# Optimization experiments

Hardware: AMD Instinct MI355X
Metric: run time of the kernel (lower is better)

Reference implementation:

```python
import jax, jax.numpy as jnp
import numpy as np


def _moving_avg(x, k):
    # Replicate-pad along channel/time axis C, then stride-1 mean window of size k.
    B, C, H, W = x.shape
    p = (k - 1) // 2
    xf = x.reshape(B, C, H * W)
    front = jnp.repeat(xf[:, :1, :], p, axis=1)
    end = jnp.repeat(xf[:, -1:, :], p, axis=1)
    padded = jnp.concatenate([front, xf, end], axis=1)  # [B, C+2p, HW]
    # Windowed mean via exclusive cumsum: sum over window i..i+k-1 = cs[i+k]-cs[i]
    cs = jnp.cumsum(padded, axis=1)
    cs = jnp.concatenate([jnp.zeros_like(cs[:, :1, :]), cs], axis=1)  # [B, C+2p+1, HW]
    out = (cs[:, k:, :] - cs[:, :-k, :]) / k  # [B, C, HW] since k odd
    return out.reshape(B, C, H, W)


def _seasonality(x, period):
    # Mean over channels sharing the same phase (c mod period), broadcast back.
    # Requires C % period == 0 (groups equal-size, matching the torch loop).
    B, C, H, W = x.shape
    G = C // period
    xr = x.reshape(B, G, period, H, W)  # [b, group, phase, h, w]
    m = jnp.mean(xr, axis=1, keepdims=True)  # [B, 1, period, H, W]
    return jnp.broadcast_to(m, (B, G, period, H, W)).reshape(B, C, H, W)


def setup_inputs() -> dict:
    key = jax.random.key(0)
    x = jax.random.normal(key, (32, 336, 32, 32), dtype=jnp.float32)
    return {"x": x, "kernel_size": 25, "pe": 24}


def reference(x, kernel_size, pe):
    T = _moving_avg(x, kernel_size)          # trend
    xd = x - T                               # detrended
    S = _seasonality(xd, pe)                 # seasonal component
    R = xd - S                               # residual
    return (T, S, R)
```

## Files before the change

### kernel.cpp

```cpp
#include <hip/hip_runtime.h>


#define C_TOT 336
#define HWSZ 1024
#define PERIOD 24
#define GROUPS 14
#define PAD 12
#define W 32
#define SEG_C 12
#define NSEG 28
#define NTHREADS (NSEG * W)

__global__ __launch_bounds__(NTHREADS, 8) void decomp_kernel(
    const float* __restrict__ x,
    float* __restrict__ outT,
    float* __restrict__ outS,
    float* __restrict__ outR)
{
    __shared__ float sx[C_TOT][W];
    __shared__ float sv[PERIOD][W];

    const int tid = threadIdx.x;
    const int b   = blockIdx.y;
    const int hw0 = blockIdx.x * W;

    const float4* __restrict__ xg =
        (const float4*)(x + (size_t)b * C_TOT * HWSZ + hw0);
    float4* __restrict__ sx4 = (float4*)sx;
    #pragma unroll
    for (int k = 0; k < 3; ++k) {
        const int idx = tid + k * NTHREADS;
        sx4[idx] = xg[(idx >> 3) * (HWSZ / 4) + (idx & 7)];
    }
    __syncthreads();

    const int col = tid & (W - 1);
    const int seg = tid >> 5;
    const int c0  = seg * SEG_C;
    const float inv25 = 1.0f / 25.0f;
    const float inv14 = 1.0f / (float)GROUPS;

    const size_t base = (size_t)b * C_TOT * HWSZ + hw0 + col;
    float* __restrict__ Tb = outT + base;
    float* __restrict__ Sb = outS + base;
    float* __restrict__ Rb = outR + base;

    float wa = 0.0f, wb = 0.0f;
    #pragma unroll
    for (int d = -PAD; d <= PAD; d += 2) {
        int cc = c0 + d;
        cc = cc < 0 ? 0 : cc; cc = cc > C_TOT - 1 ? C_TOT - 1 : cc;
        wa += sx[cc][col];
    }
    #pragma unroll
    for (int d = -PAD + 1; d <= PAD; d += 2) {
        int cc = c0 + d;
        cc = cc < 0 ? 0 : cc; cc = cc > C_TOT - 1 ? C_TOT - 1 : cc;
        wb += sx[cc][col];
    }
    float winsum = wa + wb;

    float xd[SEG_C];
    #pragma unroll
    for (int j = 0; j < SEG_C; ++j) {
        const int c = c0 + j;
        const float tval = winsum * inv25;
        __builtin_nontemporal_store(tval, &Tb[(size_t)c * HWSZ]);
        xd[j] = sx[c][col] - tval;
        int chi = c + 1 + PAD; chi = chi > C_TOT - 1 ? C_TOT - 1 : chi;
        int clo = c - PAD;     clo = clo < 0 ? 0 : clo;
        winsum += sx[chi][col] - sx[clo][col];
    }
    __syncthreads();

    #pragma unroll
    for (int j = 0; j < SEG_C; ++j) sx[c0 + j][col] = xd[j];
    __syncthreads();

    if (tid < PERIOD * W) {
        const int p = tid >> 5, cc = tid & (W - 1);
        float s = 0.0f;
        #pragma unroll
        for (int g = 0; g < GROUPS; ++g) s += sx[g * PERIOD + p][cc];
        sv[p][cc] = s * inv14;
    }
    __syncthreads();

    const int pbase = (seg & 1) * SEG_C;
    #pragma unroll
    for (int j = 0; j < SEG_C; ++j) {
        const int c = c0 + j;
        const float s = sv[pbase + j][col];
        __builtin_nontemporal_store(s, &Sb[(size_t)c * HWSZ]);
        __builtin_nontemporal_store(xd[j] - s, &Rb[(size_t)c * HWSZ]);
    }
}

extern "C" void kernel_launch(void* const* d_in, const int* in_sizes, int n_in,
                              void* d_out, int out_size, void* d_ws, size_t ws_size,
                              hipStream_t stream) {
    const float* x = (const float*)d_in[0];
    float* out = (float*)d_out;
    const size_t N = (size_t)32 * C_TOT * HWSZ;

    dim3 grid(HWSZ / W, 32);
    decomp_kernel<<<grid, NTHREADS, 0, stream>>>(x, out, out + N, out + 2 * N);
}
```

Before: 174.7 us.

## Stream input from global in two passes instead of staging tile in LDS

Drops the 336x32 shared-memory tile and uses wider 128-column blocks with 4 channel segments. Each thread reads x directly from global memory in two passes: one computes the trend and accumulates per-phase detrended sums in shared memory, and a second recomputes the trend and writes the seasonal and residual outputs. This removes the large LDS footprint so more blocks can be resident per CU. The cost is re-reading the input from global/L2 several times over: three loads per channel per pass plus the window prologue.

```diff
diff --git a/kernel.cpp b/kernel.cpp
--- a/kernel.cpp
+++ b/kernel.cpp
@@ -1,98 +1,122 @@
 #include <hip/hip_runtime.h>
 
 
-#define C_TOT 336
-#define HWSZ 1024
-#define PERIOD 24
-#define GROUPS 14
-#define PAD 12
-#define W 32
-#define SEG_C 12
-#define NSEG 28
+#define C_TOT   336
+#define HWSZ    1024
+#define PERIOD  24
+#define GROUPS  14
+#define PAD     12
+#define KWIN    25
+#define W       128
+#define NSEG    4
+#define SEG_C   (C_TOT / NSEG)
 #define NTHREADS (NSEG * W)
+#define NCHUNK  12
+#define NU      (SEG_C / NCHUNK)
 
-__global__ __launch_bounds__(NTHREADS, 8) void decomp_kernel(
+__global__ __launch_bounds__(NTHREADS) void decomp_kernel(
     const float* __restrict__ x,
     float* __restrict__ outT,
     float* __restrict__ outS,
     float* __restrict__ outR)
 {
-    __shared__ float sx[C_TOT][W];
-    __shared__ float sv[PERIOD][W];
+    __shared__ float sv[NSEG][PERIOD][W];
+    __shared__ float sS[PERIOD][W];
 
     const int tid = threadIdx.x;
+    const int h   = tid & (W - 1);
+    const int s   = tid >> 7;
     const int b   = blockIdx.y;
     const int hw0 = blockIdx.x * W;
-
-    const float4* __restrict__ xg =
-        (const float4*)(x + (size_t)b * C_TOT * HWSZ + hw0);
-    float4* __restrict__ sx4 = (float4*)sx;
-    #pragma unroll
-    for (int k = 0; k < 3; ++k) {
-        const int idx = tid + k * NTHREADS;
-        sx4[idx] = xg[(idx >> 3) * (HWSZ / 4) + (idx & 7)];
-    }
-    __syncthreads();
-
-    const int col = tid & (W - 1);
-    const int seg = tid >> 5;
-    const int c0  = seg * SEG_C;
-    const float inv25 = 1.0f / 25.0f;
+    const int c0  = s * SEG_C;
+    const float inv25 = 1.0f / (float)KWIN;
     const float inv14 = 1.0f / (float)GROUPS;
 
-    const size_t base = (size_t)b * C_TOT * HWSZ + hw0 + col;
-    float* __restrict__ Tb = outT + base;
-    float* __restrict__ Sb = outS + base;
-    float* __restrict__ Rb = outR + base;
+    const size_t base = (size_t)b * C_TOT * HWSZ + hw0 + h;
+    const float* __restrict__ xb = x    + base;
+    float* __restrict__ Tb       = outT + base;
+    float* __restrict__ Sb       = outS + base;
+    float* __restrict__ Rb       = outR + base;
 
-    float wa = 0.0f, wb = 0.0f;
     #pragma unroll
-    for (int d = -PAD; d <= PAD; d += 2) {
-        int cc = c0 + d;
-        cc = cc < 0 ? 0 : cc; cc = cc > C_TOT - 1 ? C_TOT - 1 : cc;
-        wa += sx[cc][col];
-    }
-    #pragma unroll
-    for (int d = -PAD + 1; d <= PAD; d += 2) {
-        int cc = c0 + d;
-        cc = cc < 0 ? 0 : cc; cc = cc > C_TOT - 1 ? C_TOT - 1 : cc;
-        wb += sx[cc][col];
-    }
-    float winsum = wa + wb;
+    for (int p = 0; p < PERIOD; ++p) sv[s][p][h] = 0.0f;
 
-    float xd[SEG_C];
-    #pragma unroll
-    for (int j = 0; j < SEG_C; ++j) {
-        const int c = c0 + j;
-        const float tval = winsum * inv25;
-        __builtin_nontemporal_store(tval, &Tb[(size_t)c * HWSZ]);
-        xd[j] = sx[c][col] - tval;
-        int chi = c + 1 + PAD; chi = chi > C_TOT - 1 ? C_TOT - 1 : chi;
-        int clo = c - PAD;     clo = clo < 0 ? 0 : clo;
-        winsum += sx[chi][col] - sx[clo][col];
+    {
+        float winsum = 0.0f;
+        #pragma unroll
+        for (int d = -PAD; d <= PAD; ++d) {
+            int cc = c0 + d;
+            cc = cc < 0 ? 0 : (cc > C_TOT - 1 ? C_TOT - 1 : cc);
+            winsum += xb[(size_t)cc * HWSZ];
+        }
+        int p = (s & 1) * PAD;
+        for (int u = 0; u < NU; ++u) {
+            float lead[NCHUNK], xc[NCHUNK], trail[NCHUNK];
+            #pragma unroll
+            for (int i = 0; i < NCHUNK; ++i) {
+                const int c   = c0 + u * NCHUNK + i;
+                const int chi = (c + 1 + PAD > C_TOT - 1) ? C_TOT - 1 : c + 1 + PAD;
+                const int clo = (c - PAD < 0) ? 0 : c - PAD;
+                lead[i]  = xb[(size_t)chi * HWSZ];
+                trail[i] = xb[(size_t)clo * HWSZ];
+                xc[i]    = xb[(size_t)c   * HWSZ];
+            }
+            #pragma unroll
+            for (int i = 0; i < NCHUNK; ++i) {
+                const int c = c0 + u * NCHUNK + i;
+                const float tval = winsum * inv25;
+                const float xd   = xc[i] - tval;
+                __builtin_nontemporal_store(tval, &Tb[(size_t)c * HWSZ]);
+                sv[s][p][h] += xd;
+                winsum += lead[i] - trail[i];
+                p = (p == PERIOD - 1) ? 0 : p + 1;
+            }
+        }
     }
     __syncthreads();
 
     #pragma unroll
-    for (int j = 0; j < SEG_C; ++j) sx[c0 + j][col] = xd[j];
-    __syncthreads();
-
-    if (tid < PERIOD * W) {
-        const int p = tid >> 5, cc = tid & (W - 1);
-        float s = 0.0f;
-        #pragma unroll
-        for (int g = 0; g < GROUPS; ++g) s += sx[g * PERIOD + p][cc];
-        sv[p][cc] = s * inv14;
+    for (int k = 0; k < (PERIOD * W) / NTHREADS; ++k) {
+        const int idx = tid + k * NTHREADS;
+        const int pp  = idx >> 7;
+        const int hh  = idx & (W - 1);
+        sS[pp][hh] = (sv[0][pp][hh] + sv[1][pp][hh] +
+                      sv[2][pp][hh] + sv[3][pp][hh]) * inv14;
     }
     __syncthreads();
 
-    const int pbase = (seg & 1) * SEG_C;
-    #pragma unroll
-    for (int j = 0; j < SEG_C; ++j) {
-        const int c = c0 + j;
-        const float s = sv[pbase + j][col];
-        __builtin_nontemporal_store(s, &Sb[(size_t)c * HWSZ]);
-        __builtin_nontemporal_store(xd[j] - s, &Rb[(size_t)c * HWSZ]);
+    {
+        float winsum = 0.0f;
+        #pragma unroll
+        for (int d = -PAD; d <= PAD; ++d) {
+            int cc = c0 + d;
+            cc = cc < 0 ? 0 : (cc > C_TOT - 1 ? C_TOT - 1 : cc);
+            winsum += xb[(size_t)cc * HWSZ];
+        }
+        int p = (s & 1) * PAD;
+        for (int u = 0; u < NU; ++u) {
+            float lead[NCHUNK], xc[NCHUNK], trail[NCHUNK];
+            #pragma unroll
+            for (int i = 0; i < NCHUNK; ++i) {
+                const int c   = c0 + u * NCHUNK + i;
+                const int chi = (c + 1 + PAD > C_TOT - 1) ? C_TOT - 1 : c + 1 + PAD;
+                const int clo = (c - PAD < 0) ? 0 : c - PAD;
+                lead[i]  = xb[(size_t)chi * HWSZ];
+                trail[i] = xb[(size_t)clo * HWSZ];
+                xc[i]    = xb[(size_t)c   * HWSZ];
+            }
+            #pragma unroll
+            for (int i = 0; i < NCHUNK; ++i) {
+                const int c = c0 + u * NCHUNK + i;
+                const float tval = winsum * inv25;
+                const float xd   = xc[i] - tval;
+                const float sval = sS[p][h];
+                __builtin_nontemporal_store(sval,      &Sb[(size_t)c * HWSZ]);
+                __builtin_nontemporal_store(xd - sval, &Rb[(size_t)c * HWSZ]);
+                winsum += lead[i] - trail[i];
+                p = (p == PERIOD - 1) ? 0 : p + 1;
+            }
+        }
     }
 }
 
```

After: 181.4 us. 3.8% more time.
